# Optimization experiments

Measured on AMD Instinct MI355X. Metric: run time of the kernel, lower is better.

Reference implementation:

```python
import jax, jax.numpy as jnp
import numpy as np

B, S, E, H = 2, 2048, 1024, 16
D = E // H  # head_dim = 64


def setup_inputs() -> dict:
    key = jax.random.key(0)
    k1, k2, k3 = jax.random.split(key, 3)
    scale = 0.02  # GPT-2 init scale
    return {
        "hidden_states": jax.random.normal(k1, (B, S, E), dtype=jnp.float32),
        "c_attn_w": jax.random.normal(k2, (E, 3 * E), dtype=jnp.float32) * scale,
        "c_attn_b": jnp.zeros((3 * E,), dtype=jnp.float32),
        "c_proj_w": jax.random.normal(k3, (E, E), dtype=jnp.float32) * scale,
        "c_proj_b": jnp.zeros((E,), dtype=jnp.float32),
    }


def reference(hidden_states, c_attn_w, c_attn_b, c_proj_w, c_proj_b):
    # Conv1D: x @ W + b  -> qkv [B, S, 3E]
    qkv = hidden_states @ c_attn_w + c_attn_b
    q, k, v = jnp.split(qkv, 3, axis=-1)

    # split heads -> [B, H, S, D]
    def split_heads(t):
        return t.reshape(B, S, H, D).transpose(0, 2, 1, 3)

    q, k, v = split_heads(q), split_heads(k), split_heads(v)

    # naive full attention: QK^T / sqrt(D) -> softmax -> @ V
    attn_weights = jnp.einsum("bhqd,bhkd->bhqk", q, k) / jnp.sqrt(
        jnp.asarray(D, dtype=q.dtype)
    )
    attn_weights = jax.nn.softmax(attn_weights, axis=-1)
    attn_output = jnp.einsum("bhqk,bhkd->bhqd", attn_weights, v)

    # merge heads -> [B, S, E], then output projection
    attn_output = attn_output.transpose(0, 2, 1, 3).reshape(B, S, E)
    attn_output = attn_output @ c_proj_w + c_proj_b
    return attn_output
```

## Files before the change

### kernel.cpp

```cpp
#include <hip/hip_runtime.h>

#define SEQ 2048
#define EMB 1024
#define KDIM 1024
#define CF 0.180336880111113f

typedef __attribute__((ext_vector_type(8))) short short8_t;
typedef __attribute__((ext_vector_type(4))) float floatx4;
typedef __attribute__((ext_vector_type(4))) unsigned short ushort4_t;
typedef __attribute__((ext_vector_type(4))) unsigned int uivec4;

#define GLOAD16(gp, lp)                                                        \
  __builtin_amdgcn_global_load_lds(                                            \
      (const __attribute__((address_space(1))) void*)(gp),                     \
      (__attribute__((address_space(3))) void*)(lp), 16, 0, 0)

#define WGBAR()                                   \
  do {                                            \
    __asm__ __volatile__("" ::: "memory");        \
    __builtin_amdgcn_s_barrier();                 \
    __asm__ __volatile__("" ::: "memory");        \
  } while (0)

static __device__ __forceinline__ unsigned short f2bf(float x) {
  unsigned int u = __float_as_uint(x);
  return (unsigned short)((u + 0x7fffu + ((u >> 16) & 1u)) >> 16);
}

static __device__ __forceinline__ short8_t mk_pb(unsigned int a, unsigned int b,
                                                 unsigned int c, unsigned int d) {
  uivec4 t;
  t[0] = a; t[1] = b; t[2] = c; t[3] = d;
  return __builtin_bit_cast(short8_t, t);
}

static __device__ __forceinline__ void tconv_tile(
    const float* __restrict__ W, unsigned short* __restrict__ T, int N, int K,
    int n0, int k0, int tid) {
  __shared__ float Tl[64][65];
  const int lx = tid & 15, ly = tid >> 4;
#pragma unroll
  for (int u = 0; u < 4; ++u) {
    int r = u * 16 + ly;
    float4 v = *(const float4*)&W[(size_t)(k0 + r) * N + n0 + lx * 4];
    Tl[r][lx * 4 + 0] = v.x;
    Tl[r][lx * 4 + 1] = v.y;
    Tl[r][lx * 4 + 2] = v.z;
    Tl[r][lx * 4 + 3] = v.w;
  }
  __syncthreads();
#pragma unroll
  for (int u = 0; u < 4; ++u) {
    int n = u * 16 + ly;
    ushort4_t h;
#pragma unroll
    for (int v = 0; v < 4; ++v) h[v] = f2bf(Tl[lx * 4 + v][n]);
    *(ushort4_t*)&T[(size_t)(n0 + n) * K + k0 + lx * 4] = h;
  }
}

__global__ __launch_bounds__(256) void prep(
    const float* __restrict__ hs, const float* __restrict__ caw,
    const float* __restrict__ cpw, unsigned short* __restrict__ hsb,
    unsigned short* __restrict__ w1t, unsigned short* __restrict__ w2t) {
  const int bid = blockIdx.x, tid = threadIdx.x;
  if (bid < 4096) {
    const int i = bid * 256 + tid;
    float4 v = *(const float4*)&hs[(size_t)i * 4];
    ushort4_t h = {f2bf(v.x), f2bf(v.y), f2bf(v.z), f2bf(v.w)};
    *(ushort4_t*)&hsb[(size_t)i * 4] = h;
  } else if (bid < 4864) {
    const int idx = bid - 4096;
    tconv_tile(caw, w1t, 3 * EMB, EMB, (idx % 48) * 64, (idx / 48) * 64, tid);
  } else {
    const int idx = bid - 4864;
    tconv_tile(cpw, w2t, EMB, EMB, (idx % 16) * 64, (idx / 16) * 64, tid);
  }
}

template <int MODE, int BN>
__global__ __launch_bounds__(256) void gemm_pl(
    const unsigned short* __restrict__ Ag, const unsigned short* __restrict__ Bg,
    const float* __restrict__ bias, float* __restrict__ outF,
    unsigned short* __restrict__ qk, unsigned short* __restrict__ vt) {
  __shared__ __attribute__((aligned(16))) unsigned short Ah[3][128 * 32];
  __shared__ __attribute__((aligned(16))) unsigned short Bh[3][BN * 32];
  const int NJ = BN / 32;

  const int tid = threadIdx.x;
  const int w = tid >> 6, lane = tid & 63;
  const int quad = lane >> 4, c = lane & 15;

  int bm, bn;
  {
    const int L = blockIdx.x, x = L & 7, g = L >> 3;
    if (MODE == 0) {
      bm = ((x & 1) * 16 + (g & 15)) * 128;
      bn = ((x >> 1) * 6 + (g >> 4)) * 128;
    } else {
      bm = ((x & 3) * 8 + (g & 7)) * 128;
      bn = ((x >> 2) * 8 + (g >> 3)) * 64;
    }
  }
  const int wm = (w >> 1) * 64, wn = (w & 1) * (BN / 2);

  const unsigned short* gsrc = (w < 2) ? Ag : Bg;
  const int lbo = (w < 2) ? (w & 1) * 64 * 32 : (w & 1) * (BN / 2) * 32;
  const int rbase = (w < 2) ? (bm + (w & 1) * 64) : (bn + (w & 1) * (BN / 2));
  const int nloads = (w < 2) ? 4 : (BN / 32);
  const int srow = lane >> 2;
  const int sblk = (lane & 3) ^ ((lane >> 3) & 3);
  const char* gp0 = (const char*)(gsrc + (size_t)(rbase + srow) * KDIM) + sblk * 16;

  floatx4 acc[4][NJ];
  const floatx4 z = {0.f, 0.f, 0.f, 0.f};
#pragma unroll
  for (int i = 0; i < 4; ++i)
#pragma unroll
    for (int j = 0; j < NJ; ++j) acc[i][j] = z;

  const int sw = (c >> 1) & 3;

#define STAGE_G(buf, kt)                                                       \
  do {                                                                         \
    unsigned short* ld = ((w < 2) ? Ah[buf] : Bh[buf]) + lbo;                  \
    const char* gp = gp0 + (size_t)(kt) * 64;                                  \
    for (int i_ = 0; i_ < nloads; ++i_)                                        \
      GLOAD16(gp + (size_t)i_ * 16 * (KDIM * 2), &ld[i_ * 512]);               \
  } while (0)

  STAGE_G(0, 0);
  STAGE_G(1, 1);

  for (int t = 0; t < 32; ++t) {
    if (BN == 128 || w < 2) {
      __asm__ __volatile__("s_waitcnt vmcnt(4)" ::: "memory");
    } else {
      __asm__ __volatile__("s_waitcnt vmcnt(2)" ::: "memory");
    }
    WGBAR();
    STAGE_G((t + 2) % 3, (t + 2) & 31);
    const unsigned short* Ac = Ah[t % 3];
    const unsigned short* Bc = Bh[t % 3];

    const int oct = (quad ^ sw) * 8;
    short8_t a[4], b[NJ];
#pragma unroll
    for (int i = 0; i < 4; ++i)
      a[i] = *(const short8_t*)&Ac[(wm + 16 * i + c) * 32 + oct];
#pragma unroll
    for (int j = 0; j < NJ; ++j)
      b[j] = *(const short8_t*)&Bc[(wn + 16 * j + c) * 32 + oct];
#pragma unroll
    for (int i = 0; i < 4; ++i)
#pragma unroll
      for (int j = 0; j < NJ; ++j)
        acc[i][j] = __builtin_amdgcn_mfma_f32_16x16x32_bf16(b[j], a[i], acc[i][j], 0, 0, 0);
  }
#undef STAGE_G

  __asm__ __volatile__("s_waitcnt vmcnt(0)" ::: "memory");

#pragma unroll
  for (int i = 0; i < 4; ++i) {
    const int row = bm + wm + 16 * i + c;
#pragma unroll
    for (int j = 0; j < NJ; ++j) {
      const int col0 = bn + wn + 16 * j + quad * 4;
      floatx4 v = acc[i][j] + *(const floatx4*)&bias[col0];
      if (MODE == 0) {
        if (col0 < 1024) v = v * CF;
        if (col0 < 2048) {
          ushort4_t pk = {f2bf(v[0]), f2bf(v[1]), f2bf(v[2]), f2bf(v[3])};
          *(ushort4_t*)&qk[(size_t)row * 2048 + col0] = pk;
        } else {
          const int c2 = col0 - 2048, hh = c2 >> 6, d0 = c2 & 63;
          const int bb = row >> 11, s = row & 2047;
          const int j = s & 63;
          const int lam = (j & 0x20) | ((j & 0x0C) << 1) | ((j & 0x10) >> 2) | (j & 3);
          const int sp = (s & ~63) | lam;
          unsigned short* vb = &vt[((size_t)(bb * 16 + hh) * 64 + d0) * 2048 + sp];
          vb[0 * 2048] = f2bf(v[0]);
          vb[1 * 2048] = f2bf(v[1]);
          vb[2 * 2048] = f2bf(v[2]);
          vb[3 * 2048] = f2bf(v[3]);
        }
      } else {
        *(floatx4*)&outF[(size_t)row * 1024 + col0] = v;
      }
    }
  }
}

static __device__ __forceinline__ void stage_kv(
    int w, int srow, int sblkg, const unsigned short* __restrict__ gK,
    const unsigned short* __restrict__ gV, unsigned short* Kbuf,
    unsigned short* Vbuf, int jt) {
  if (w < 2) {
    const unsigned short* g0 = gK + (size_t)(jt * 64 + w * 32 + srow) * 2048 + sblkg * 8;
    unsigned short* l0 = &Kbuf[(w * 32) * 64];
#pragma unroll
    for (int i = 0; i < 4; ++i) GLOAD16(g0 + (size_t)i * 8 * 2048, &l0[i * 512]);
  } else {
    const unsigned short* g0 = gV + (size_t)((w - 2) * 32 + srow) * 2048 + jt * 64 + sblkg * 8;
    unsigned short* l0 = &Vbuf[((w - 2) * 32) * 64];
#pragma unroll
    for (int i = 0; i < 4; ++i) GLOAD16(g0 + (size_t)i * 8 * 2048, &l0[i * 512]);
  }
}

__global__ __launch_bounds__(256) void attn6(
    const unsigned short* __restrict__ qk, const unsigned short* __restrict__ vt,
    unsigned short* __restrict__ ao) {
  __shared__ __attribute__((aligned(16))) unsigned short Ks[3][64 * 64];
  __shared__ __attribute__((aligned(16))) unsigned short Vs[3][64 * 64];

  const int tid = threadIdx.x;
  const int w = tid >> 6, lane = tid & 63, quad = lane >> 4, c = lane & 15;
  const int q0 = blockIdx.x * 128, h = blockIdx.y, b = blockIdx.z;
  const int rk = c & 7;

  short8_t qf[2][2];
  {
    const size_t rb = (size_t)b * SEQ + q0 + w * 32;
#pragma unroll
    for (int mi = 0; mi < 2; ++mi) {
      const size_t qr = (rb + mi * 16 + c) * 2048 + h * 64 + quad * 8;
      qf[mi][0] = *(const short8_t*)&qk[qr];
      qf[mi][1] = *(const short8_t*)&qk[qr + 32];
    }
  }
  __asm__ __volatile__("s_waitcnt vmcnt(0)" ::: "memory");

  floatx4 O[2][4], Osum[2];
  const floatx4 z = {0.f, 0.f, 0.f, 0.f};
#pragma unroll
  for (int mi = 0; mi < 2; ++mi) {
    Osum[mi] = z;
#pragma unroll
    for (int dg = 0; dg < 4; ++dg) O[mi][dg] = z;
  }
  short8_t ones;
#pragma unroll
  for (int e = 0; e < 8; ++e) ones[e] = (short)0x3F80;

  const int srow = lane >> 3;
  const int sblkg = (lane & 7) ^ srow;
  const unsigned short* gK = qk + (size_t)b * SEQ * 2048 + 1024 + h * 64;
  const unsigned short* gV = vt + (size_t)(b * 16 + h) * 64 * 2048;

  stage_kv(w, srow, sblkg, gK, gV, Ks[0], Vs[0], 0);
  stage_kv(w, srow, sblkg, gK, gV, Ks[1], Vs[1], 1);

  for (int t = 0; t < 32; ++t) {
    __asm__ __volatile__("s_waitcnt vmcnt(4)" ::: "memory");
    WGBAR();
    stage_kv(w, srow, sblkg, gK, gV, Ks[(t + 2) % 3], Vs[(t + 2) % 3], (t + 2) & 31);
    const unsigned short* Kc = Ks[t % 3];
    const unsigned short* Vc = Vs[t % 3];

    floatx4 S[2][4];
#pragma unroll
    for (int mi = 0; mi < 2; ++mi)
#pragma unroll
      for (int jg = 0; jg < 4; ++jg) S[mi][jg] = z;
#pragma unroll
    for (int kd = 0; kd < 2; ++kd) {
      const int oct = ((4 * kd + quad) ^ rk) * 8;
#pragma unroll
      for (int jg = 0; jg < 4; ++jg) {
        short8_t kf = *(const short8_t*)&Kc[(jg * 16 + c) * 64 + oct];
#pragma unroll
        for (int mi = 0; mi < 2; ++mi)
          S[mi][jg] = __builtin_amdgcn_mfma_f32_16x16x32_bf16(kf, qf[mi][kd], S[mi][jg], 0, 0, 0);
      }
    }

    unsigned int pw[2][4][2];
#pragma unroll
    for (int mi = 0; mi < 2; ++mi)
#pragma unroll
      for (int jg = 0; jg < 4; ++jg) {
        float p0 = __builtin_amdgcn_exp2f(S[mi][jg][0]);
        float p1 = __builtin_amdgcn_exp2f(S[mi][jg][1]);
        float p2 = __builtin_amdgcn_exp2f(S[mi][jg][2]);
        float p3 = __builtin_amdgcn_exp2f(S[mi][jg][3]);
        pw[mi][jg][0] = (__float_as_uint(p1) & 0xFFFF0000u) | (__float_as_uint(p0) >> 16);
        pw[mi][jg][1] = (__float_as_uint(p3) & 0xFFFF0000u) | (__float_as_uint(p2) >> 16);
      }

#pragma unroll
    for (int kq = 0; kq < 2; ++kq) {
      const int oct = ((4 * kq + quad) ^ rk) * 8;
      short8_t pb[2];
#pragma unroll
      for (int mi = 0; mi < 2; ++mi) {
        pb[mi] = mk_pb(pw[mi][2 * kq][0], pw[mi][2 * kq][1],
                       pw[mi][2 * kq + 1][0], pw[mi][2 * kq + 1][1]);
        Osum[mi] = __builtin_amdgcn_mfma_f32_16x16x32_bf16(ones, pb[mi], Osum[mi], 0, 0, 0);
      }
#pragma unroll
      for (int dg = 0; dg < 4; ++dg) {
        short8_t vf = *(const short8_t*)&Vc[(dg * 16 + c) * 64 + oct];
#pragma unroll
        for (int mi = 0; mi < 2; ++mi)
          O[mi][dg] = __builtin_amdgcn_mfma_f32_16x16x32_bf16(vf, pb[mi], O[mi][dg], 0, 0, 0);
      }
    }
  }

  __asm__ __volatile__("s_waitcnt vmcnt(0)" ::: "memory");

#pragma unroll
  for (int mi = 0; mi < 2; ++mi) {
    const float inv = 1.0f / Osum[mi][0];
    const size_t row = (size_t)b * SEQ + q0 + w * 32 + mi * 16 + c;
#pragma unroll
    for (int dg = 0; dg < 4; ++dg) {
      ushort4_t ov = {f2bf(O[mi][dg][0] * inv), f2bf(O[mi][dg][1] * inv),
                      f2bf(O[mi][dg][2] * inv), f2bf(O[mi][dg][3] * inv)};
      *(ushort4_t*)&ao[row * EMB + h * 64 + dg * 16 + quad * 4] = ov;
    }
  }
}

extern "C" void kernel_launch(void* const* d_in, const int* in_sizes, int n_in,
                              void* d_out, int out_size, void* d_ws, size_t ws_size,
                              hipStream_t stream) {
  const float* hs = (const float*)d_in[0];
  const float* c_attn_w = (const float*)d_in[1];
  const float* c_attn_b = (const float*)d_in[2];
  const float* c_proj_w = (const float*)d_in[3];
  const float* c_proj_b = (const float*)d_in[4];
  float* out = (float*)d_out;

  char* ws = (char*)d_ws;
  unsigned short* hsb = (unsigned short*)(ws + 0);
  unsigned short* qk  = (unsigned short*)(ws + 8388608);
  unsigned short* vt  = (unsigned short*)(ws + 25165824);
  unsigned short* aob = (unsigned short*)(ws + 33554432);
  unsigned short* w1t = (unsigned short*)(ws + 41943040);
  unsigned short* w2t = (unsigned short*)(ws + 48234496);

  prep<<<5120, 256, 0, stream>>>(hs, c_attn_w, c_proj_w, hsb, w1t, w2t);
  gemm_pl<0, 128><<<768, 256, 0, stream>>>(hsb, w1t, c_attn_b, nullptr, qk, vt);
  attn6<<<dim3(16, 16, 2), 256, 0, stream>>>(qk, vt, aob);
  gemm_pl<2, 64><<<512, 256, 0, stream>>>(aob, w2t, c_proj_b, out, nullptr, nullptr);
}
```

Measured before the change: 181.0 us.

## Split attention key tile across wave pairs and reduce partial outputs via LDS

Changes the attention kernel's work split. Previously each of 4 waves owned 32 query rows across all 64 keys of a tile. Now wave pairs share 64 query rows and each wave takes half of the key tile, so each K/V fragment loaded from LDS feeds 4 query sub-tiles instead of 2. The two partial O and rowsum accumulators are combined through shared memory at the end. It also swaps the bf16 pack mask/shift for a single v_perm. This costs more accumulator registers (O grows to 4x4) and an extra epilogue reduction with barriers.

New measurement: 176.1 us. -2.7%, faster.

```diff
diff --git a/kernel.cpp b/kernel.cpp
--- a/kernel.cpp
+++ b/kernel.cpp
@@ -32,6 +32,11 @@
   uivec4 t;
   t[0] = a; t[1] = b; t[2] = c; t[3] = d;
   return __builtin_bit_cast(short8_t, t);
+}
+
+static __device__ __forceinline__ unsigned int pack_bf(float p0, float p1) {
+  return __builtin_amdgcn_perm(__float_as_uint(p1), __float_as_uint(p0),
+                               0x07060302u);
 }
 
 static __device__ __forceinline__ void tconv_tile(
@@ -209,22 +214,24 @@
   }
 }
 
-__global__ __launch_bounds__(256) void attn6(
+__global__ __launch_bounds__(256) void attn7(
     const unsigned short* __restrict__ qk, const unsigned short* __restrict__ vt,
     unsigned short* __restrict__ ao) {
-  __shared__ __attribute__((aligned(16))) unsigned short Ks[3][64 * 64];
-  __shared__ __attribute__((aligned(16))) unsigned short Vs[3][64 * 64];
+  __shared__ __attribute__((aligned(16))) unsigned short SMEM[6 * 4096];
+  unsigned short* Ksb = SMEM;
+  unsigned short* Vsb = SMEM + 3 * 4096;
 
   const int tid = threadIdx.x;
   const int w = tid >> 6, lane = tid & 63, quad = lane >> 4, c = lane & 15;
+  const int qh = w >> 1, kh = w & 1;
   const int q0 = blockIdx.x * 128, h = blockIdx.y, b = blockIdx.z;
   const int rk = c & 7;
 
-  short8_t qf[2][2];
+  short8_t qf[4][2];
   {
-    const size_t rb = (size_t)b * SEQ + q0 + w * 32;
-#pragma unroll
-    for (int mi = 0; mi < 2; ++mi) {
+    const size_t rb = (size_t)b * SEQ + q0 + qh * 64;
+#pragma unroll
+    for (int mi = 0; mi < 4; ++mi) {
       const size_t qr = (rb + mi * 16 + c) * 2048 + h * 64 + quad * 8;
       qf[mi][0] = *(const short8_t*)&qk[qr];
       qf[mi][1] = *(const short8_t*)&qk[qr + 32];
@@ -232,10 +239,10 @@
   }
   __asm__ __volatile__("s_waitcnt vmcnt(0)" ::: "memory");
 
-  floatx4 O[2][4], Osum[2];
+  floatx4 O[4][4], Osum[4];
   const floatx4 z = {0.f, 0.f, 0.f, 0.f};
 #pragma unroll
-  for (int mi = 0; mi < 2; ++mi) {
+  for (int mi = 0; mi < 4; ++mi) {
     Osum[mi] = z;
 #pragma unroll
     for (int dg = 0; dg < 4; ++dg) O[mi][dg] = z;
@@ -249,77 +256,94 @@
   const unsigned short* gK = qk + (size_t)b * SEQ * 2048 + 1024 + h * 64;
   const unsigned short* gV = vt + (size_t)(b * 16 + h) * 64 * 2048;
 
-  stage_kv(w, srow, sblkg, gK, gV, Ks[0], Vs[0], 0);
-  stage_kv(w, srow, sblkg, gK, gV, Ks[1], Vs[1], 1);
+  stage_kv(w, srow, sblkg, gK, gV, Ksb, Vsb, 0);
+  stage_kv(w, srow, sblkg, gK, gV, Ksb + 4096, Vsb + 4096, 1);
 
   for (int t = 0; t < 32; ++t) {
     __asm__ __volatile__("s_waitcnt vmcnt(4)" ::: "memory");
     WGBAR();
-    stage_kv(w, srow, sblkg, gK, gV, Ks[(t + 2) % 3], Vs[(t + 2) % 3], (t + 2) & 31);
-    const unsigned short* Kc = Ks[t % 3];
-    const unsigned short* Vc = Vs[t % 3];
-
-    floatx4 S[2][4];
-#pragma unroll
-    for (int mi = 0; mi < 2; ++mi)
-#pragma unroll
-      for (int jg = 0; jg < 4; ++jg) S[mi][jg] = z;
+    stage_kv(w, srow, sblkg, gK, gV, Ksb + ((t + 2) % 3) * 4096,
+             Vsb + ((t + 2) % 3) * 4096, (t + 2) & 31);
+    const unsigned short* Kc = Ksb + (t % 3) * 4096;
+    const unsigned short* Vc = Vsb + (t % 3) * 4096;
+
+    floatx4 S[4][2];
+#pragma unroll
+    for (int mi = 0; mi < 4; ++mi)
+#pragma unroll
+      for (int jg = 0; jg < 2; ++jg) S[mi][jg] = z;
 #pragma unroll
     for (int kd = 0; kd < 2; ++kd) {
       const int oct = ((4 * kd + quad) ^ rk) * 8;
 #pragma unroll
-      for (int jg = 0; jg < 4; ++jg) {
-        short8_t kf = *(const short8_t*)&Kc[(jg * 16 + c) * 64 + oct];
-#pragma unroll
-        for (int mi = 0; mi < 2; ++mi)
+      for (int jg = 0; jg < 2; ++jg) {
+        short8_t kf = *(const short8_t*)&Kc[((kh * 2 + jg) * 16 + c) * 64 + oct];
+#pragma unroll
+        for (int mi = 0; mi < 4; ++mi)
           S[mi][jg] = __builtin_amdgcn_mfma_f32_16x16x32_bf16(kf, qf[mi][kd], S[mi][jg], 0, 0, 0);
       }
     }
 
-    unsigned int pw[2][4][2];
-#pragma unroll
-    for (int mi = 0; mi < 2; ++mi)
-#pragma unroll
-      for (int jg = 0; jg < 4; ++jg) {
+    unsigned int pw[4][2][2];
+#pragma unroll
+    for (int mi = 0; mi < 4; ++mi)
+#pragma unroll
+      for (int jg = 0; jg < 2; ++jg) {
         float p0 = __builtin_amdgcn_exp2f(S[mi][jg][0]);
         float p1 = __builtin_amdgcn_exp2f(S[mi][jg][1]);
         float p2 = __builtin_amdgcn_exp2f(S[mi][jg][2]);
         float p3 = __builtin_amdgcn_exp2f(S[mi][jg][3]);
-        pw[mi][jg][0] = (__float_as_uint(p1) & 0xFFFF0000u) | (__float_as_uint(p0) >> 16);
-        pw[mi][jg][1] = (__float_as_uint(p3) & 0xFFFF0000u) | (__float_as_uint(p2) >> 16);
+        pw[mi][jg][0] = pack_bf(p0, p1);
+        pw[mi][jg][1] = pack_bf(p2, p3);
       }
 
-#pragma unroll
-    for (int kq = 0; kq < 2; ++kq) {
-      const int oct = ((4 * kq + quad) ^ rk) * 8;
-      short8_t pb[2];
-#pragma unroll
-      for (int mi = 0; mi < 2; ++mi) {
-        pb[mi] = mk_pb(pw[mi][2 * kq][0], pw[mi][2 * kq][1],
-                       pw[mi][2 * kq + 1][0], pw[mi][2 * kq + 1][1]);
-        Osum[mi] = __builtin_amdgcn_mfma_f32_16x16x32_bf16(ones, pb[mi], Osum[mi], 0, 0, 0);
+    const int octv = ((4 * kh + quad) ^ rk) * 8;
+    short8_t pb[4];
+#pragma unroll
+    for (int mi = 0; mi < 4; ++mi) {
+      pb[mi] = mk_pb(pw[mi][0][0], pw[mi][0][1], pw[mi][1][0], pw[mi][1][1]);
+      Osum[mi] = __builtin_amdgcn_mfma_f32_16x16x32_bf16(ones, pb[mi], Osum[mi], 0, 0, 0);
+    }
+#pragma unroll
+    for (int dg = 0; dg < 4; ++dg) {
+      short8_t vf = *(const short8_t*)&Vc[(dg * 16 + c) * 64 + octv];
+#pragma unroll
+      for (int mi = 0; mi < 4; ++mi)
+        O[mi][dg] = __builtin_amdgcn_mfma_f32_16x16x32_bf16(vf, pb[mi], O[mi][dg], 0, 0, 0);
+    }
+  }
+
+  __asm__ __volatile__("s_waitcnt vmcnt(0)" ::: "memory");
+  WGBAR();
+
+  float* Of = (float*)SMEM;
+  float* Ss = (float*)(SMEM + 17408);
+  if (kh == 1) {
+#pragma unroll
+    for (int mi = 0; mi < 4; ++mi) {
+      const int row = mi * 16 + c;
+      float* orow = &Of[(qh * 64 + row) * 68];
+#pragma unroll
+      for (int dg = 0; dg < 4; ++dg)
+        *(floatx4*)&orow[dg * 16 + quad * 4] = O[mi][dg];
+      if (quad == 0) Ss[qh * 64 + row] = Osum[mi][0];
+    }
+  }
+  WGBAR();
+  if (kh == 0) {
+#pragma unroll
+    for (int mi = 0; mi < 4; ++mi) {
+      const int row = mi * 16 + c;
+      const float inv = 1.0f / (Osum[mi][0] + Ss[qh * 64 + row]);
+      const float* orow = &Of[(qh * 64 + row) * 68];
+      const size_t grow = (size_t)b * SEQ + q0 + qh * 64 + row;
+#pragma unroll
+      for (int dg = 0; dg < 4; ++dg) {
+        floatx4 o = O[mi][dg] + *(const floatx4*)&orow[dg * 16 + quad * 4];
+        ushort4_t ov = {f2bf(o[0] * inv), f2bf(o[1] * inv),
+                        f2bf(o[2] * inv), f2bf(o[3] * inv)};
+        *(ushort4_t*)&ao[grow * EMB + h * 64 + dg * 16 + quad * 4] = ov;
       }
-#pragma unroll
-      for (int dg = 0; dg < 4; ++dg) {
-        short8_t vf = *(const short8_t*)&Vc[(dg * 16 + c) * 64 + oct];
-#pragma unroll
-        for (int mi = 0; mi < 2; ++mi)
-          O[mi][dg] = __builtin_amdgcn_mfma_f32_16x16x32_bf16(vf, pb[mi], O[mi][dg], 0, 0, 0);
-      }
-    }
-  }
-
-  __asm__ __volatile__("s_waitcnt vmcnt(0)" ::: "memory");
-
-#pragma unroll
-  for (int mi = 0; mi < 2; ++mi) {
-    const float inv = 1.0f / Osum[mi][0];
-    const size_t row = (size_t)b * SEQ + q0 + w * 32 + mi * 16 + c;
-#pragma unroll
-    for (int dg = 0; dg < 4; ++dg) {
-      ushort4_t ov = {f2bf(O[mi][dg][0] * inv), f2bf(O[mi][dg][1] * inv),
-                      f2bf(O[mi][dg][2] * inv), f2bf(O[mi][dg][3] * inv)};
-      *(ushort4_t*)&ao[row * EMB + h * 64 + dg * 16 + quad * 4] = ov;
     }
   }
 }
@@ -344,6 +368,6 @@
 
   prep<<<5120, 256, 0, stream>>>(hs, c_attn_w, c_proj_w, hsb, w1t, w2t);
   gemm_pl<0, 128><<<768, 256, 0, stream>>>(hsb, w1t, c_attn_b, nullptr, qk, vt);
-  attn6<<<dim3(16, 16, 2), 256, 0, stream>>>(qk, vt, aob);
+  attn7<<<dim3(16, 16, 2), 256, 0, stream>>>(qk, vt, aob);
   gemm_pl<2, 64><<<512, 256, 0, stream>>>(aob, w2t, c_proj_b, out, nullptr, nullptr);
 }
```

## Split attention over key halves with smaller query tiles and a combine pass

Applied to the files above, without the earlier changes.

The attention kernel now gives each block 64 queries and half of the key sequence, processed in 32-key tiles with double buffering instead of triple. This raises the grid from 512 to 2048 blocks, so more work is available to fill the GPU. Each half writes a normalized bf16 partial output and its row sums into reused workspace, and a new combine kernel merges the halves by weighting each with its share of the summed exponentials. In exchange it adds an extra kernel launch, extra global traffic for the partial outputs, and a second bf16 rounding of the attention output.

Result: slower. 193.3 us (+6.8%).

```diff
diff --git a/kernel.cpp b/kernel.cpp
--- a/kernel.cpp
+++ b/kernel.cpp
@@ -27,11 +27,20 @@
   return (unsigned short)((u + 0x7fffu + ((u >> 16) & 1u)) >> 16);
 }
 
+static __device__ __forceinline__ float bf2f(short v) {
+  return __uint_as_float(((unsigned int)(unsigned short)v) << 16);
+}
+
 static __device__ __forceinline__ short8_t mk_pb(unsigned int a, unsigned int b,
                                                  unsigned int c, unsigned int d) {
   uivec4 t;
   t[0] = a; t[1] = b; t[2] = c; t[3] = d;
   return __builtin_bit_cast(short8_t, t);
+}
+
+static __device__ __forceinline__ unsigned int pack_bf(float p0, float p1) {
+  return __builtin_amdgcn_perm(__float_as_uint(p1), __float_as_uint(p0),
+                               0x07060302u);
 }
 
 static __device__ __forceinline__ void tconv_tile(
@@ -192,136 +201,142 @@
   }
 }
 
-static __device__ __forceinline__ void stage_kv(
-    int w, int srow, int sblkg, const unsigned short* __restrict__ gK,
-    const unsigned short* __restrict__ gV, unsigned short* Kbuf,
-    unsigned short* Vbuf, int jt) {
+static __device__ __forceinline__ void stage_kv32(
+    int w, int lane, const unsigned short* __restrict__ gKb,
+    const unsigned short* __restrict__ gVb, unsigned short* Kbuf,
+    unsigned short* Vbuf, int t) {
   if (w < 2) {
-    const unsigned short* g0 = gK + (size_t)(jt * 64 + w * 32 + srow) * 2048 + sblkg * 8;
-    unsigned short* l0 = &Kbuf[(w * 32) * 64];
-#pragma unroll
-    for (int i = 0; i < 4; ++i) GLOAD16(g0 + (size_t)i * 8 * 2048, &l0[i * 512]);
+    const int srow = lane >> 3;
+    const int sblk = (lane & 7) ^ srow;
+    const unsigned short* g0 =
+        gKb + (size_t)(t * 32 + w * 16 + srow) * 2048 + sblk * 8;
+    unsigned short* l0 = &Kbuf[(w * 16) * 64];
+    GLOAD16(g0, l0);
+    GLOAD16(g0 + (size_t)8 * 2048, l0 + 8 * 64);
   } else {
-    const unsigned short* g0 = gV + (size_t)((w - 2) * 32 + srow) * 2048 + jt * 64 + sblkg * 8;
-    unsigned short* l0 = &Vbuf[((w - 2) * 32) * 64];
-#pragma unroll
-    for (int i = 0; i < 4; ++i) GLOAD16(g0 + (size_t)i * 8 * 2048, &l0[i * 512]);
-  }
-}
-
-__global__ __launch_bounds__(256) void attn6(
+    const int srow = lane >> 2;
+    const int sblk = (lane & 3) ^ (srow & 3);
+    const unsigned short* g0 =
+        gVb + (size_t)((w - 2) * 32 + srow) * 2048 + t * 32 + sblk * 8;
+    unsigned short* l0 = &Vbuf[((w - 2) * 32) * 32];
+    GLOAD16(g0, l0);
+    GLOAD16(g0 + (size_t)16 * 2048, l0 + 16 * 32);
+  }
+}
+
+__global__ __launch_bounds__(256, 8) void attn8b(
     const unsigned short* __restrict__ qk, const unsigned short* __restrict__ vt,
-    unsigned short* __restrict__ ao) {
-  __shared__ __attribute__((aligned(16))) unsigned short Ks[3][64 * 64];
-  __shared__ __attribute__((aligned(16))) unsigned short Vs[3][64 * 64];
+    unsigned short* __restrict__ p0, unsigned short* __restrict__ p1,
+    float* __restrict__ ssum) {
+  __shared__ __attribute__((aligned(16))) unsigned short SMEM[8192];
+  unsigned short* Ksb = SMEM;
+  unsigned short* Vsb = SMEM + 4096;
 
   const int tid = threadIdx.x;
   const int w = tid >> 6, lane = tid & 63, quad = lane >> 4, c = lane & 15;
-  const int q0 = blockIdx.x * 128, h = blockIdx.y, b = blockIdx.z;
-  const int rk = c & 7;
-
-  short8_t qf[2][2];
+  const int L = blockIdx.x, x = L & 7, g = L >> 3;
+  const int hb = x * 4 + (g >> 6);
+  const int h = hb & 15, b = hb >> 4;
+  const int q0 = ((g >> 1) & 31) * 64;
+  const int half = g & 1;
+  const int rk = c & 7, rk2 = c & 3;
+
+  short8_t qf[2];
   {
-    const size_t rb = (size_t)b * SEQ + q0 + w * 32;
-#pragma unroll
-    for (int mi = 0; mi < 2; ++mi) {
-      const size_t qr = (rb + mi * 16 + c) * 2048 + h * 64 + quad * 8;
-      qf[mi][0] = *(const short8_t*)&qk[qr];
-      qf[mi][1] = *(const short8_t*)&qk[qr + 32];
-    }
+    const size_t qr =
+        ((size_t)(b * SEQ + q0 + w * 16 + c)) * 2048 + h * 64 + quad * 8;
+    qf[0] = *(const short8_t*)&qk[qr];
+    qf[1] = *(const short8_t*)&qk[qr + 32];
   }
   __asm__ __volatile__("s_waitcnt vmcnt(0)" ::: "memory");
 
-  floatx4 O[2][4], Osum[2];
+  floatx4 O[4], Osum;
   const floatx4 z = {0.f, 0.f, 0.f, 0.f};
-#pragma unroll
-  for (int mi = 0; mi < 2; ++mi) {
-    Osum[mi] = z;
-#pragma unroll
-    for (int dg = 0; dg < 4; ++dg) O[mi][dg] = z;
-  }
+  Osum = z;
+#pragma unroll
+  for (int dg = 0; dg < 4; ++dg) O[dg] = z;
   short8_t ones;
 #pragma unroll
   for (int e = 0; e < 8; ++e) ones[e] = (short)0x3F80;
 
-  const int srow = lane >> 3;
-  const int sblkg = (lane & 7) ^ srow;
-  const unsigned short* gK = qk + (size_t)b * SEQ * 2048 + 1024 + h * 64;
-  const unsigned short* gV = vt + (size_t)(b * 16 + h) * 64 * 2048;
-
-  stage_kv(w, srow, sblkg, gK, gV, Ks[0], Vs[0], 0);
-  stage_kv(w, srow, sblkg, gK, gV, Ks[1], Vs[1], 1);
+  const unsigned short* gKb =
+      qk + ((size_t)b * SEQ + half * 1024) * 2048 + 1024 + h * 64;
+  const unsigned short* gVb =
+      vt + (size_t)(b * 16 + h) * 64 * 2048 + half * 1024;
+
+  stage_kv32(w, lane, gKb, gVb, Ksb, Vsb, 0);
 
   for (int t = 0; t < 32; ++t) {
-    __asm__ __volatile__("s_waitcnt vmcnt(4)" ::: "memory");
+    __asm__ __volatile__("s_waitcnt vmcnt(0)" ::: "memory");
     WGBAR();
-    stage_kv(w, srow, sblkg, gK, gV, Ks[(t + 2) % 3], Vs[(t + 2) % 3], (t + 2) & 31);
-    const unsigned short* Kc = Ks[t % 3];
-    const unsigned short* Vc = Vs[t % 3];
-
-    floatx4 S[2][4];
-#pragma unroll
-    for (int mi = 0; mi < 2; ++mi)
-#pragma unroll
-      for (int jg = 0; jg < 4; ++jg) S[mi][jg] = z;
+    if (t < 31)
+      stage_kv32(w, lane, gKb, gVb, Ksb + ((t + 1) & 1) * 2048,
+                 Vsb + ((t + 1) & 1) * 2048, t + 1);
+    const unsigned short* Kc = Ksb + (t & 1) * 2048;
+    const unsigned short* Vc = Vsb + (t & 1) * 2048;
+
+    floatx4 S[2];
+    S[0] = z; S[1] = z;
 #pragma unroll
     for (int kd = 0; kd < 2; ++kd) {
       const int oct = ((4 * kd + quad) ^ rk) * 8;
 #pragma unroll
-      for (int jg = 0; jg < 4; ++jg) {
+      for (int jg = 0; jg < 2; ++jg) {
         short8_t kf = *(const short8_t*)&Kc[(jg * 16 + c) * 64 + oct];
-#pragma unroll
-        for (int mi = 0; mi < 2; ++mi)
-          S[mi][jg] = __builtin_amdgcn_mfma_f32_16x16x32_bf16(kf, qf[mi][kd], S[mi][jg], 0, 0, 0);
+        S[jg] = __builtin_amdgcn_mfma_f32_16x16x32_bf16(kf, qf[kd], S[jg], 0, 0, 0);
       }
     }
 
-    unsigned int pw[2][4][2];
-#pragma unroll
-    for (int mi = 0; mi < 2; ++mi)
-#pragma unroll
-      for (int jg = 0; jg < 4; ++jg) {
-        float p0 = __builtin_amdgcn_exp2f(S[mi][jg][0]);
-        float p1 = __builtin_amdgcn_exp2f(S[mi][jg][1]);
-        float p2 = __builtin_amdgcn_exp2f(S[mi][jg][2]);
-        float p3 = __builtin_amdgcn_exp2f(S[mi][jg][3]);
-        pw[mi][jg][0] = (__float_as_uint(p1) & 0xFFFF0000u) | (__float_as_uint(p0) >> 16);
-        pw[mi][jg][1] = (__float_as_uint(p3) & 0xFFFF0000u) | (__float_as_uint(p2) >> 16);
-      }
-
-#pragma unroll
-    for (int kq = 0; kq < 2; ++kq) {
-      const int oct = ((4 * kq + quad) ^ rk) * 8;
-      short8_t pb[2];
-#pragma unroll
-      for (int mi = 0; mi < 2; ++mi) {
-        pb[mi] = mk_pb(pw[mi][2 * kq][0], pw[mi][2 * kq][1],
-                       pw[mi][2 * kq + 1][0], pw[mi][2 * kq + 1][1]);
-        Osum[mi] = __builtin_amdgcn_mfma_f32_16x16x32_bf16(ones, pb[mi], Osum[mi], 0, 0, 0);
-      }
-#pragma unroll
-      for (int dg = 0; dg < 4; ++dg) {
-        short8_t vf = *(const short8_t*)&Vc[(dg * 16 + c) * 64 + oct];
-#pragma unroll
-        for (int mi = 0; mi < 2; ++mi)
-          O[mi][dg] = __builtin_amdgcn_mfma_f32_16x16x32_bf16(vf, pb[mi], O[mi][dg], 0, 0, 0);
-      }
-    }
-  }
-
-  __asm__ __volatile__("s_waitcnt vmcnt(0)" ::: "memory");
-
-#pragma unroll
-  for (int mi = 0; mi < 2; ++mi) {
-    const float inv = 1.0f / Osum[mi][0];
-    const size_t row = (size_t)b * SEQ + q0 + w * 32 + mi * 16 + c;
+    unsigned int pw[2][2];
+#pragma unroll
+    for (int jg = 0; jg < 2; ++jg) {
+      float pe0 = __builtin_amdgcn_exp2f(S[jg][0]);
+      float pe1 = __builtin_amdgcn_exp2f(S[jg][1]);
+      float pe2 = __builtin_amdgcn_exp2f(S[jg][2]);
+      float pe3 = __builtin_amdgcn_exp2f(S[jg][3]);
+      pw[jg][0] = pack_bf(pe0, pe1);
+      pw[jg][1] = pack_bf(pe2, pe3);
+    }
+
+    short8_t pb = mk_pb(pw[0][0], pw[0][1], pw[1][0], pw[1][1]);
+    Osum = __builtin_amdgcn_mfma_f32_16x16x32_bf16(ones, pb, Osum, 0, 0, 0);
 #pragma unroll
     for (int dg = 0; dg < 4; ++dg) {
-      ushort4_t ov = {f2bf(O[mi][dg][0] * inv), f2bf(O[mi][dg][1] * inv),
-                      f2bf(O[mi][dg][2] * inv), f2bf(O[mi][dg][3] * inv)};
-      *(ushort4_t*)&ao[row * EMB + h * 64 + dg * 16 + quad * 4] = ov;
-    }
-  }
+      short8_t vf = *(const short8_t*)&Vc[(dg * 16 + c) * 32 + (quad ^ rk2) * 8];
+      O[dg] = __builtin_amdgcn_mfma_f32_16x16x32_bf16(vf, pb, O[dg], 0, 0, 0);
+    }
+  }
+
+  const float inv = 1.0f / Osum[0];
+  unsigned short* P = half ? p1 : p0;
+  const size_t rowb =
+      ((size_t)(b * SEQ + q0 + w * 16 + c)) * 1024 + h * 64;
+#pragma unroll
+  for (int dg = 0; dg < 4; ++dg) {
+    ushort4_t ov = {f2bf(O[dg][0] * inv), f2bf(O[dg][1] * inv),
+                    f2bf(O[dg][2] * inv), f2bf(O[dg][3] * inv)};
+    *(ushort4_t*)&P[rowb + dg * 16 + quad * 4] = ov;
+  }
+  if (quad == 0)
+    ssum[half * 65536 + ((b * 16 + h) << 11) + q0 + w * 16 + c] = Osum[0];
+}
+
+__global__ __launch_bounds__(256) void comb(
+    const unsigned short* __restrict__ p0, unsigned short* p1ao,
+    const float* __restrict__ ssum) {
+  const int e = (blockIdx.x * 256 + threadIdx.x) * 8;
+  const int br = e >> 6, h = br & 15, bs = br >> 4;
+  const int sidx = (((bs >> 11) * 16 + h) << 11) | (bs & 2047);
+  const float s0 = ssum[sidx], s1 = ssum[65536 + sidx];
+  const float r = 1.0f / (s0 + s1);
+  const float w0 = s0 * r, w1 = s1 * r;
+  short8_t a = *(const short8_t*)&p0[e];
+  short8_t bb = *(const short8_t*)&p1ao[e];
+  short8_t res;
+#pragma unroll
+  for (int j = 0; j < 8; ++j)
+    res[j] = (short)f2bf(bf2f(a[j]) * w0 + bf2f(bb[j]) * w1);
+  *(short8_t*)&p1ao[e] = res;
 }
 
 extern "C" void kernel_launch(void* const* d_in, const int* in_sizes, int n_in,
@@ -341,9 +356,11 @@
   unsigned short* aob = (unsigned short*)(ws + 33554432);
   unsigned short* w1t = (unsigned short*)(ws + 41943040);
   unsigned short* w2t = (unsigned short*)(ws + 48234496);
+  float* ssum = (float*)(ws + 41943040);
 
   prep<<<5120, 256, 0, stream>>>(hs, c_attn_w, c_proj_w, hsb, w1t, w2t);
   gemm_pl<0, 128><<<768, 256, 0, stream>>>(hsb, w1t, c_attn_b, nullptr, qk, vt);
-  attn6<<<dim3(16, 16, 2), 256, 0, stream>>>(qk, vt, aob);
+  attn8b<<<2048, 256, 0, stream>>>(qk, vt, hsb, aob, ssum);
+  comb<<<2048, 256, 0, stream>>>(hsb, aob, ssum);
   gemm_pl<2, 64><<<512, 256, 0, stream>>>(aob, w2t, c_proj_b, out, nullptr, nullptr);
 }
```
